# Kernel tuning notes

Measured on AMD Instinct MI355X. Metric: run time of the kernel, lower is better.

The kernel has to match this reference:

```python
import jax, jax.numpy as jnp
import numpy as np

KERNEL_SIZE = 3


def setup_inputs() -> dict:
    key = jax.random.key(0)
    k1, k2 = jax.random.split(key)
    x = jax.random.normal(k1, (4, 64, 256, 256), dtype=jnp.float32)
    kernel = jax.random.normal(k2, (4, KERNEL_SIZE * KERNEL_SIZE, 256, 256), dtype=jnp.float32)
    return {"x": x, "kernel": kernel}


def reference(x, kernel):
    # x: [b, c, h, w]; kernel: [b, k*k, h, w]
    b, c, h, w = x.shape
    k = KERNEL_SIZE
    p = k // 2
    # nn.ReflectionPad2d(k//2)
    xp = jnp.pad(x, ((0, 0), (0, 0), (p, p), (p, p)), mode="reflect")
    # softmax over the k*k dimension (dim=1)
    kw = jax.nn.softmax(kernel, axis=1)  # [b, k*k, h, w]
    # Fused gather-multiply-reduce: instead of materializing the k^2-expanded
    # unfold tensor, accumulate over the k*k shifted views. Unfold ordering is
    # row-major over (dy, dx), matching index i = dy*k + dx.
    out = jnp.zeros_like(x)
    for dy in range(k):
        for dx in range(k):
            patch = xp[:, :, dy:dy + h, dx:dx + w]          # [b, c, h, w]
            out = out + kw[:, dy * k + dx][:, None] * patch  # broadcast over c
    return out
```

## Files before the change

kernel.cpp:

```cpp
#include <hip/hip_runtime.h>
#include <stdint.h>


constexpr int BATCH = 4;
constexpr int CHAN  = 64;
constexpr int HH    = 256;
constexpr int WW    = 256;
constexpr int CG    = 4;
constexpr int RPB   = 4;
constexpr int NROW  = RPB + 2;
constexpr int NWG   = (HH / RPB) * (CHAN / CG) * BATCH;
constexpr int NXCD  = 8;
constexpr int CPX   = NWG / NXCD;

typedef float vf4 __attribute__((ext_vector_type(4)));
typedef const __attribute__((address_space(1))) void* gas_ptr;
typedef __attribute__((address_space(3))) void* las_ptr;

__global__ __launch_bounds__(256) void dynconv_kernel(
    const float* __restrict__ x,
    const float* __restrict__ ker,
    float* __restrict__ out)
{
    __shared__ float lds[CG][NROW][WW];

    const int id   = blockIdx.x;
    const int work = (id & (NXCD - 1)) * CPX + (id >> 3);
    const int hband = work & 63;
    const int cg    = (work >> 6) & 15;
    const int b     = work >> 10;

    const int t  = threadIdx.x;
    const int rb = t >> 6;
    const int wq = t & 63;
    const int w0 = wq * 4;
    const int h0 = hband * RPB;
    const int h  = h0 + rb;

    const long cs = (long)HH * WW;
    const float* xb = x   + (((long)b * CHAN + cg * CG) * cs);
    float*       ob = out + (((long)b * CHAN + cg * CG) * cs);

    #pragma unroll
    for (int k = 0; k < (CG * NROW) / RPB; ++k) {
        const int idx  = k * RPB + rb;
        const int ch   = idx / NROW;
        const int slot = idx % NROW;
        int g = h0 - 1 + slot;
        g = (g < 0) ? 1 : ((g > HH - 1) ? HH - 2 : g);
        const float* gsrc = xb + (long)ch * cs + (long)g * WW + w0;
        __builtin_amdgcn_global_load_lds((gas_ptr)gsrc, (las_ptr)&lds[ch][slot][0], 16, 0, 0);
    }

    float kv[9][4];
    const long kbase = (((long)b * 9) * HH + h) * WW + w0;
    #pragma unroll
    for (int j = 0; j < 9; ++j) {
        const float4 v = *reinterpret_cast<const float4*>(ker + kbase + (long)j * HH * WW);
        kv[j][0] = v.x; kv[j][1] = v.y; kv[j][2] = v.z; kv[j][3] = v.w;
    }
    #pragma unroll
    for (int p = 0; p < 4; ++p) {
        float m = kv[0][p];
        #pragma unroll
        for (int j = 1; j < 9; ++j) m = fmaxf(m, kv[j][p]);
        float s = 0.f;
        #pragma unroll
        for (int j = 0; j < 9; ++j) { kv[j][p] = __expf(kv[j][p] - m); s += kv[j][p]; }
        const float inv = 1.0f / s;
        #pragma unroll
        for (int j = 0; j < 9; ++j) kv[j][p] *= inv;
    }

    __syncthreads();

    #pragma unroll
    for (int i = 0; i < CG; ++i) {
        float acc0 = 0.f, acc1 = 0.f, acc2 = 0.f, acc3 = 0.f;
        #pragma unroll
        for (int r = 0; r < 3; ++r) {
            const float4 v = *reinterpret_cast<const float4*>(&lds[i][rb + r][w0]);
            float lft = __shfl_up(v.w, 1);
            if (wq == 0)  lft = v.y;
            float rgt = __shfl_down(v.x, 1);
            if (wq == 63) rgt = v.z;
            const float vals[6] = { lft, v.x, v.y, v.z, v.w, rgt };
            #pragma unroll
            for (int dx = 0; dx < 3; ++dx) {
                const int j = r * 3 + dx;
                acc0 = fmaf(kv[j][0], vals[0 + dx], acc0);
                acc1 = fmaf(kv[j][1], vals[1 + dx], acc1);
                acc2 = fmaf(kv[j][2], vals[2 + dx], acc2);
                acc3 = fmaf(kv[j][3], vals[3 + dx], acc3);
            }
        }
        vf4 o; o.x = acc0; o.y = acc1; o.z = acc2; o.w = acc3;
        __builtin_nontemporal_store(o, reinterpret_cast<vf4*>(ob + (long)i * cs + (long)h * WW + w0));
    }
}

extern "C" void kernel_launch(void* const* d_in, const int* in_sizes, int n_in,
                              void* d_out, int out_size, void* d_ws, size_t ws_size,
                              hipStream_t stream) {
    const float* x   = (const float*)d_in[0];
    const float* ker = (const float*)d_in[1];
    float* out = (float*)d_out;

    dynconv_kernel<<<dim3(NWG), dim3(256), 0, stream>>>(x, ker, out);
}
```

Before: 27.79 us.

## Process two row bands per workgroup with double-buffered LDS staging

Each workgroup now handles two consecutive 4-row bands, which halves the grid size. While the first band is being convolved, the second band's rows are loaded into a second LDS buffer, and its softmax is computed before the second sync. The aim is to overlap global-to-LDS loads with compute and to spread launch overhead over more work. In exchange, LDS per block doubles and the extra register set for the second band's weights may lower occupancy, and the smaller grid may leave CUs underutilised.

```diff
diff --git a/kernel.cpp b/kernel.cpp
--- a/kernel.cpp
+++ b/kernel.cpp
@@ -9,7 +9,8 @@
 constexpr int CG    = 4;
 constexpr int RPB   = 4;
 constexpr int NROW  = RPB + 2;
-constexpr int NWG   = (HH / RPB) * (CHAN / CG) * BATCH;
+constexpr int NB    = 2;
+constexpr int NWG   = (HH / (RPB * NB)) * (CHAN / CG) * BATCH;
 constexpr int NXCD  = 8;
 constexpr int CPX   = NWG / NXCD;
 
@@ -22,81 +23,104 @@
     const float* __restrict__ ker,
     float* __restrict__ out)
 {
-    __shared__ float lds[CG][NROW][WW];
+    __shared__ float lds[NB][CG][NROW][WW];
 
-    const int id   = blockIdx.x;
-    const int work = (id & (NXCD - 1)) * CPX + (id >> 3);
-    const int hband = work & 63;
-    const int cg    = (work >> 6) & 15;
-    const int b     = work >> 10;
+    const int id    = blockIdx.x;
+    const int work  = (id & (NXCD - 1)) * CPX + (id >> 3);
+    const int hpair = work & 31;
+    const int cg    = (work >> 5) & 15;
+    const int b     = work >> 9;
 
     const int t  = threadIdx.x;
     const int rb = t >> 6;
     const int wq = t & 63;
     const int w0 = wq * 4;
-    const int h0 = hband * RPB;
-    const int h  = h0 + rb;
 
     const long cs = (long)HH * WW;
     const float* xb = x   + (((long)b * CHAN + cg * CG) * cs);
     float*       ob = out + (((long)b * CHAN + cg * CG) * cs);
+    const long kplane = (long)HH * WW;
+    const float* kb = ker + (long)b * 9 * kplane;
 
-    #pragma unroll
-    for (int k = 0; k < (CG * NROW) / RPB; ++k) {
-        const int idx  = k * RPB + rb;
-        const int ch   = idx / NROW;
-        const int slot = idx % NROW;
-        int g = h0 - 1 + slot;
-        g = (g < 0) ? 1 : ((g > HH - 1) ? HH - 2 : g);
-        const float* gsrc = xb + (long)ch * cs + (long)g * WW + w0;
-        __builtin_amdgcn_global_load_lds((gas_ptr)gsrc, (las_ptr)&lds[ch][slot][0], 16, 0, 0);
-    }
+    auto stage_band = [&](int buf, int h0) {
+        #pragma unroll
+        for (int k = 0; k < (CG * NROW) / RPB; ++k) {
+            const int idx  = k * RPB + rb;
+            const int ch   = idx / NROW;
+            const int slot = idx % NROW;
+            int g = h0 - 1 + slot;
+            g = (g < 0) ? 1 : ((g > HH - 1) ? HH - 2 : g);
+            const float* gsrc = xb + (long)ch * cs + (long)g * WW + w0;
+            __builtin_amdgcn_global_load_lds((gas_ptr)gsrc,
+                                             (las_ptr)&lds[buf][ch][slot][0], 16, 0, 0);
+        }
+    };
 
-    float kv[9][4];
-    const long kbase = (((long)b * 9) * HH + h) * WW + w0;
-    #pragma unroll
-    for (int j = 0; j < 9; ++j) {
-        const float4 v = *reinterpret_cast<const float4*>(ker + kbase + (long)j * HH * WW);
-        kv[j][0] = v.x; kv[j][1] = v.y; kv[j][2] = v.z; kv[j][3] = v.w;
-    }
-    #pragma unroll
-    for (int p = 0; p < 4; ++p) {
-        float m = kv[0][p];
+    auto softmax_row = [&](int h, float kv[9][4]) {
+        const long kroff = (long)h * WW + w0;
         #pragma unroll
-        for (int j = 1; j < 9; ++j) m = fmaxf(m, kv[j][p]);
-        float s = 0.f;
+        for (int j = 0; j < 9; ++j) {
+            const float4 v = *reinterpret_cast<const float4*>(kb + kroff + (long)j * kplane);
+            kv[j][0] = v.x; kv[j][1] = v.y; kv[j][2] = v.z; kv[j][3] = v.w;
+        }
         #pragma unroll
-        for (int j = 0; j < 9; ++j) { kv[j][p] = __expf(kv[j][p] - m); s += kv[j][p]; }
-        const float inv = 1.0f / s;
+        for (int p = 0; p < 4; ++p) {
+            float m = kv[0][p];
+            #pragma unroll
+            for (int j = 1; j < 9; ++j) m = fmaxf(m, kv[j][p]);
+            float s = 0.f;
+            #pragma unroll
+            for (int j = 0; j < 9; ++j) { kv[j][p] = __expf(kv[j][p] - m); s += kv[j][p]; }
+            const float inv = 1.0f / s;
+            #pragma unroll
+            for (int j = 0; j < 9; ++j) kv[j][p] *= inv;
+        }
+    };
+
+    auto conv_band = [&](int buf, int h, float kv[9][4]) {
         #pragma unroll
-        for (int j = 0; j < 9; ++j) kv[j][p] *= inv;
-    }
+        for (int i = 0; i < CG; ++i) {
+            float acc0 = 0.f, acc1 = 0.f, acc2 = 0.f, acc3 = 0.f;
+            #pragma unroll
+            for (int r = 0; r < 3; ++r) {
+                const float4 v = *reinterpret_cast<const float4*>(&lds[buf][i][rb + r][w0]);
+                float lft = __shfl_up(v.w, 1);
+                if (wq == 0)  lft = v.y;
+                float rgt = __shfl_down(v.x, 1);
+                if (wq == 63) rgt = v.z;
+                const float vals[6] = { lft, v.x, v.y, v.z, v.w, rgt };
+                #pragma unroll
+                for (int dx = 0; dx < 3; ++dx) {
+                    const int j = r * 3 + dx;
+                    acc0 = fmaf(kv[j][0], vals[0 + dx], acc0);
+                    acc1 = fmaf(kv[j][1], vals[1 + dx], acc1);
+                    acc2 = fmaf(kv[j][2], vals[2 + dx], acc2);
+                    acc3 = fmaf(kv[j][3], vals[3 + dx], acc3);
+                }
+            }
+            vf4 o; o.x = acc0; o.y = acc1; o.z = acc2; o.w = acc3;
+            __builtin_nontemporal_store(o,
+                reinterpret_cast<vf4*>(ob + (long)i * cs + (long)h * WW + w0));
+        }
+    };
 
+    const int h0a = (hpair * NB + 0) * RPB;
+    const int h0b = (hpair * NB + 1) * RPB;
+    const int ha  = h0a + rb;
+    const int hb  = h0b + rb;
+
+    float kvA[9][4], kvB[9][4];
+
+    stage_band(0, h0a);
+    softmax_row(ha, kvA);
     __syncthreads();
 
-    #pragma unroll
-    for (int i = 0; i < CG; ++i) {
-        float acc0 = 0.f, acc1 = 0.f, acc2 = 0.f, acc3 = 0.f;
-        #pragma unroll
-        for (int r = 0; r < 3; ++r) {
-            const float4 v = *reinterpret_cast<const float4*>(&lds[i][rb + r][w0]);
-            float lft = __shfl_up(v.w, 1);
-            if (wq == 0)  lft = v.y;
-            float rgt = __shfl_down(v.x, 1);
-            if (wq == 63) rgt = v.z;
-            const float vals[6] = { lft, v.x, v.y, v.z, v.w, rgt };
-            #pragma unroll
-            for (int dx = 0; dx < 3; ++dx) {
-                const int j = r * 3 + dx;
-                acc0 = fmaf(kv[j][0], vals[0 + dx], acc0);
-                acc1 = fmaf(kv[j][1], vals[1 + dx], acc1);
-                acc2 = fmaf(kv[j][2], vals[2 + dx], acc2);
-                acc3 = fmaf(kv[j][3], vals[3 + dx], acc3);
-            }
-        }
-        vf4 o; o.x = acc0; o.y = acc1; o.z = acc2; o.w = acc3;
-        __builtin_nontemporal_store(o, reinterpret_cast<vf4*>(ob + (long)i * cs + (long)h * WW + w0));
-    }
+    stage_band(1, h0b);
+    conv_band(0, ha, kvA);
+    softmax_row(hb, kvB);
+    __syncthreads();
+
+    conv_band(1, hb, kvB);
 }
 
 extern "C" void kernel_launch(void* const* d_in, const int* in_sizes, int n_in,
```

Result: slower. 33.64 us (+21.0%).
